# Optimization experiments

Measured on AMD Instinct MI355X. Metric: run time of the kernel, lower is better.

The kernel has to match this reference:

```python
import jax, jax.numpy as jnp
import numpy as np

H = 16       # num attention heads
HKV = 4      # num key/value heads
HD = 128     # head dim
EPS = 1e-6
ROPE_BASE = 10000.0


def _rms_norm(x, w):
    # per-head RMSNorm over last dim (head_dim), computed in fp32
    xf = x.astype(jnp.float32)
    var = jnp.mean(xf * xf, axis=-1, keepdims=True)
    return (w * (xf * jax.lax.rsqrt(var + EPS))).astype(x.dtype)


def _rotate_half(x):
    x1, x2 = jnp.split(x, 2, axis=-1)
    return jnp.concatenate((-x2, x1), axis=-1)


def _rope_cos_sin(position_ids, dtype):
    inv_freq = 1.0 / (ROPE_BASE ** (jnp.arange(0, HD, 2, dtype=jnp.float32) / HD))
    freqs = position_ids.astype(jnp.float32)[..., None] * inv_freq  # [B,S,HD/2]
    emb = jnp.concatenate((freqs, freqs), axis=-1)                  # [B,S,HD]
    return jnp.cos(emb).astype(dtype), jnp.sin(emb).astype(dtype)


def setup_inputs() -> dict:
    key = jax.random.key(0)
    ks = jax.random.split(key, 6)
    B, S, D = 2, 2048, 2048
    return {
        "hidden_states": jax.random.normal(ks[0], (B, S, D), jnp.float32),
        "wq": jax.random.normal(ks[1], (D, H * HD), jnp.float32) * 0.02,
        "wk": jax.random.normal(ks[2], (D, HKV * HD), jnp.float32) * 0.02,
        "wv": jax.random.normal(ks[3], (D, HKV * HD), jnp.float32) * 0.02,
        "wo": jax.random.normal(ks[4], (H * HD, D), jnp.float32) * 0.02,
        "q_norm_w": jnp.ones((HD,), jnp.float32),
        "k_norm_w": jnp.ones((HD,), jnp.float32),
        "position_ids": jnp.tile(jnp.arange(S, dtype=jnp.int32)[None, :], (B, 1)),
    }


def reference(hidden_states, wq, wk, wv, wo, q_norm_w, k_norm_w, position_ids):
    B, S, D = hidden_states.shape
    # projections + per-head q/k RMSNorm (Qwen3)
    q = _rms_norm(jnp.einsum("bsd,de->bse", hidden_states, wq).reshape(B, S, H, HD), q_norm_w)
    k = _rms_norm(jnp.einsum("bsd,de->bse", hidden_states, wk).reshape(B, S, HKV, HD), k_norm_w)
    v = jnp.einsum("bsd,de->bse", hidden_states, wv).reshape(B, S, HKV, HD)
    # [B, H, S, HD]
    q = q.transpose(0, 2, 1, 3)
    k = k.transpose(0, 2, 1, 3)
    v = v.transpose(0, 2, 1, 3)
    # RoPE (cos/sin broadcast over head dim, unsqueeze_dim=1)
    cos, sin = _rope_cos_sin(position_ids, q.dtype)
    cos, sin = cos[:, None], sin[:, None]
    q = q * cos + _rotate_half(q) * sin
    k = k * cos + _rotate_half(k) * sin
    # GQA repeat_kv: [B,HKV,S,HD] -> [B,H,S,HD]
    n_rep = H // HKV
    k = jnp.repeat(k, n_rep, axis=1)
    v = jnp.repeat(v, n_rep, axis=1)
    # SDPA, causal
    scale = 1.0 / jnp.sqrt(jnp.asarray(HD, q.dtype))
    scores = jnp.einsum("bhqd,bhkd->bhqk", q, k) * scale
    causal = jnp.tril(jnp.ones((S, S), bool))
    scores = jnp.where(causal, scores, jnp.asarray(-1e9, scores.dtype))
    attn = jax.nn.softmax(scores, axis=-1)
    out = jnp.einsum("bhqk,bhkd->bhqd", attn, v)         # [B,H,S,HD]
    out = out.transpose(0, 2, 1, 3).reshape(B, S, H * HD)
    return jnp.einsum("bse,ed->bsd", out, wo)
```

## Files before the change

kernel.cpp:

```cpp
#include <hip/hip_runtime.h>
#include <hip/hip_bf16.h>
#include <cstddef>

constexpr int B_   = 2;
constexpr int S_   = 2048;
constexpr int D_   = 2048;
constexpr int H_   = 16;
constexpr int HKV_ = 4;
constexpr int HD_  = 128;
constexpr int M_   = B_ * S_;
constexpr int NQKV_ = H_ * HD_ + 2 * HKV_ * HD_;
constexpr float QSCALE = 0.08838834764831845f;

typedef __attribute__((ext_vector_type(8))) short bs8;
typedef __attribute__((ext_vector_type(4))) float fx4;

__device__ __forceinline__ void split2(float x, short& hi, short& lo) {
  __hip_bfloat16 h = __float2bfloat16(x);
  float hf = __bfloat162float(h);
  __hip_bfloat16 l = __float2bfloat16(x - hf);
  hi = *(short*)&h;
  lo = *(short*)&l;
}

__device__ __forceinline__ void gload16(const short* g, short* l) {
  __builtin_amdgcn_global_load_lds(
      (const __attribute__((address_space(1))) void*)g,
      (__attribute__((address_space(3))) void*)l, 16, 0, 0);
}

__global__ __launch_bounds__(256) void split_hidden(
    const float4* __restrict__ X, short* __restrict__ out)
{
  const long i4  = (long)blockIdx.x * 256 + threadIdx.x;
  const long row = i4 >> 9;
  const long c   = (i4 & 511) * 4;
  const float4 v = X[i4];
  short h[4], l[4];
  split2(v.x, h[0], l[0]); split2(v.y, h[1], l[1]);
  split2(v.z, h[2], l[2]); split2(v.w, h[3], l[3]);
  *(short4*)&out[row * 4096 + c]        = make_short4(h[0], h[1], h[2], h[3]);
  *(short4*)&out[row * 4096 + 2048 + c] = make_short4(l[0], l[1], l[2], l[3]);
}

__global__ __launch_bounds__(256) void tsplit(
    const float* __restrict__ W, int N, short* __restrict__ out, int row0)
{
  __shared__ float tile[32][33];
  const int k0 = blockIdx.y * 32;
  const int n0 = blockIdx.x * 32;
  const int x = threadIdx.x, y = threadIdx.y;
  #pragma unroll
  for (int i = 0; i < 4; ++i)
    tile[y + 8 * i][x] = W[(size_t)(k0 + y + 8 * i) * N + n0 + x];
  __syncthreads();
  #pragma unroll
  for (int i = 0; i < 4; ++i) {
    const int n = n0 + y + 8 * i;
    const float v = tile[x][y + 8 * i];
    short hi, lo;
    split2(v, hi, lo);
    out[(size_t)(row0 + n) * 4096 + k0 + x]        = hi;
    out[(size_t)(row0 + n) * 4096 + 2048 + k0 + x] = lo;
  }
}

__global__ __launch_bounds__(256, 2) void gemm_split_bf16(
    const short* __restrict__ Asp, const short* __restrict__ Bsp,
    float* __restrict__ C, int M, int N, int K)
{
  __shared__ short As[128 * 32];
  __shared__ short Bs[128 * 32];

  const int t    = threadIdx.x;
  const int lane = t & 63, wid = t >> 6;
  const int wr   = wid >> 1, wc = wid & 1;
  const int bm   = blockIdx.y * 128, bn = blockIdx.x * 128;
  const int ld   = 2 * K;

  fx4 acc[4][4] = {};

  const int sr = t >> 2;
  const int sk = (t & 3) * 8;
  short* lA  = As + t * 8;
  short* lA2 = As + (t + 256) * 8;
  short* lB  = Bs + t * 8;
  short* lB2 = Bs + (t + 256) * 8;
  const short* gA = Asp + (size_t)(bm + sr) * ld + sk;
  const short* gB = Bsp + (size_t)(bn + sr) * ld + sk;
  const size_t rstep = (size_t)64 * ld;

  const int lr = lane & 15, lk = (lane >> 4) * 8;

  for (int kp = 0; kp < 3 * K; kp += 32) {
    const int ca = (kp < 2 * K) ? kp : kp - 2 * K;
    const int cb = (kp < K) ? kp : kp - K;
    gload16(gA + ca, lA);
    gload16(gA + ca + rstep, lA2);
    gload16(gB + cb, lB);
    gload16(gB + cb + rstep, lB2);
    __syncthreads();

    bs8 af[4], bf[4];
    #pragma unroll
    for (int m = 0; m < 4; ++m)
      af[m] = *(const bs8*)&As[(wr * 64 + m * 16 + lr) * 32 + lk];
    #pragma unroll
    for (int n = 0; n < 4; ++n)
      bf[n] = *(const bs8*)&Bs[(wc * 64 + n * 16 + lr) * 32 + lk];
    #pragma unroll
    for (int m = 0; m < 4; ++m)
      #pragma unroll
      for (int n = 0; n < 4; ++n)
        acc[m][n] = __builtin_amdgcn_mfma_f32_16x16x32_bf16(af[m], bf[n], acc[m][n], 0, 0, 0);
    __syncthreads();
  }

  const int lg = lane >> 4;
  #pragma unroll
  for (int m = 0; m < 4; ++m)
    #pragma unroll
    for (int n = 0; n < 4; ++n) {
      const int col = bn + wc * 64 + n * 16 + lr;
      #pragma unroll
      for (int r = 0; r < 4; ++r) {
        const int row = bm + wr * 64 + m * 16 + lg * 4 + r;
        C[(size_t)row * N + col] = acc[m][n][r];
      }
    }
}

__global__ __launch_bounds__(64) void rmsrope(
    float* __restrict__ qkv, const float* __restrict__ qw,
    const float* __restrict__ kw, const int* __restrict__ pos_ids)
{
  const int row  = blockIdx.x;
  const int lane = threadIdx.x;
  constexpr int NQROWS = M_ * H_;
  const bool isq = row < NQROWS;

  int token; float* ptr; const float* w;
  if (isq) {
    token = row / H_;
    ptr = qkv + (size_t)token * NQKV_ + (row % H_) * HD_;
    w = qw;
  } else {
    const int rk = row - NQROWS;
    token = rk / HKV_;
    ptr = qkv + (size_t)token * NQKV_ + 2048 + (rk % HKV_) * HD_;
    w = kw;
  }

  const float x1 = ptr[lane];
  const float x2 = ptr[lane + 64];
  float ss = x1 * x1 + x2 * x2;
  #pragma unroll
  for (int m = 1; m < 64; m <<= 1) ss += __shfl_xor(ss, m, 64);
  const float rinv = rsqrtf(ss * (1.0f / 128.0f) + 1e-6f);
  const float y1 = x1 * rinv * w[lane];
  const float y2 = x2 * rinv * w[lane + 64];

  const int pos = pos_ids[token];
  const float f = (float)pos * powf(10000.0f, -(float)lane * (1.0f / 64.0f));
  float sn, c;
  sincosf(f, &sn, &c);
  const float o1 = y1 * c - y2 * sn;
  const float o2 = y2 * c + y1 * sn;

  if (isq) {
    ptr[lane]      = o1;
    ptr[lane + 64] = o2;
  } else {
    short* srow = (short*)ptr;
    short h1, l1, h2, l2;
    split2(o1, h1, l1);
    split2(o2, h2, l2);
    srow[lane]       = h1;  srow[lane + 64]  = h2;
    srow[128 + lane] = l1;  srow[192 + lane] = l2;
  }
}

__global__ __launch_bounds__(256) void vtrans(
    const float* __restrict__ qkv, short* __restrict__ vsp)
{
  __shared__ float tile[32][33];
  const int by = blockIdx.y;
  const int b = by >> 4, kvh = (by >> 2) & 3, d0 = (by & 3) * 32;
  const int s0 = blockIdx.x * 32;
  const int tx = threadIdx.x, ty = threadIdx.y;
  #pragma unroll
  for (int i = 0; i < 4; ++i)
    tile[ty + 8 * i][tx] =
        qkv[(size_t)(b * S_ + s0 + ty + 8 * i) * NQKV_ + 2560 + kvh * 128 + d0 + tx];
  __syncthreads();
  #pragma unroll
  for (int i = 0; i < 4; ++i) {
    const int d = d0 + ty + 8 * i;
    __hip_bfloat16 v = __float2bfloat16(tile[tx][ty + 8 * i]);
    vsp[((size_t)(b * HKV_ + kvh) * 128 + d) * (size_t)S_ + s0 + tx] = *(short*)&v;
  }
}

__global__ __launch_bounds__(256, 2) void attn_mfma(
    const float* __restrict__ qkv, const short* __restrict__ vsp,
    short* __restrict__ osp)
{
  __shared__ __align__(16) short Kh[64 * 128];
  __shared__ __align__(16) short Kl[64 * 128];
  __shared__ __align__(16) short Vt[128 * 64];
  __shared__ __align__(16) short sP[64 * 64];

  const int t    = threadIdx.x;
  const int lane = t & 63;
  const int w    = t >> 6;
  const int lr   = lane & 15;
  const int g    = lane >> 4;
  const int qt = blockIdx.x, bh = blockIdx.y;
  const int b = bh >> 4, h = bh & 15;
  const int kvh = h >> 2;
  const int q0  = qt * 64;
  const int bhk = b * HKV_ + kvh;
  const short* kb = (const short*)qkv;

  bs8 qh[4], ql[4];
  {
    const float* qrow = qkv + (size_t)(b * S_ + q0 + 16 * w + lr) * NQKV_ + h * HD_ + g * 8;
    #pragma unroll
    for (int dc = 0; dc < 4; ++dc) {
      float x[8];
      *(float4*)&x[0] = *(const float4*)(qrow + 32 * dc);
      *(float4*)&x[4] = *(const float4*)(qrow + 32 * dc + 4);
      #pragma unroll
      for (int i = 0; i < 8; ++i) {
        short hi, lo;
        split2(x[i] * QSCALE, hi, lo);
        qh[dc][i] = hi; ql[dc][i] = lo;
      }
    }
  }

  fx4 o[8] = {};
  float m_i[4] = {-1e30f, -1e30f, -1e30f, -1e30f};
  float l_i[4] = {0.f, 0.f, 0.f, 0.f};

  const int sj = t >> 2, sq = t & 3;
  const int vd = t >> 1, vjh = t & 1;

  for (int kt = 0; kt <= qt; ++kt) {
    const int k0 = kt * 64;
    __syncthreads();

    {
      const short* krow = kb + (size_t)(b * S_ + k0 + sj) * 6144 + 4096 + kvh * 256 + 32 * sq;
      const short* vrow = vsp + ((size_t)bhk * 128 + vd) * (size_t)S_ + k0 + 32 * vjh;
      #pragma unroll
      for (int ci = 0; ci < 4; ++ci) {
        const int kblk = (((4 * sq + ci) ^ (sj & 15)) << 3);
        *(bs8*)&Kh[sj * 128 + kblk] = *(const bs8*)(krow + 8 * ci);
        *(bs8*)&Kl[sj * 128 + kblk] = *(const bs8*)(krow + 128 + 8 * ci);
        *(bs8*)&Vt[vd * 64 + ((((4 * vjh + ci) ^ (vd & 7))) << 3)] = *(const bs8*)(vrow + 8 * ci);
      }
    }
    __syncthreads();

    fx4 s[4] = {};
    #pragma unroll
    for (int dc = 0; dc < 4; ++dc) {
      #pragma unroll
      for (int n = 0; n < 4; ++n) {
        const int ko = (16 * n + lr) * 128 + (((dc * 4 + g) ^ lr) << 3);
        const bs8 fh = *(const bs8*)&Kh[ko];
        const bs8 fl = *(const bs8*)&Kl[ko];
        s[n] = __builtin_amdgcn_mfma_f32_16x16x32_bf16(qh[dc], fh, s[n], 0, 0, 0);
        s[n] = __builtin_amdgcn_mfma_f32_16x16x32_bf16(ql[dc], fh, s[n], 0, 0, 0);
        s[n] = __builtin_amdgcn_mfma_f32_16x16x32_bf16(qh[dc], fl, s[n], 0, 0, 0);
      }
    }

    if (kt == qt) {
      #pragma unroll
      for (int n = 0; n < 4; ++n)
        #pragma unroll
        for (int r = 0; r < 4; ++r)
          if (16 * n + lr > 16 * w + 4 * g + r) s[n][r] = -1e30f;
    }

    #pragma unroll
    for (int r = 0; r < 4; ++r) {
      float rm = fmaxf(fmaxf(s[0][r], s[1][r]), fmaxf(s[2][r], s[3][r]));
      rm = fmaxf(rm, __shfl_xor(rm, 1, 64));
      rm = fmaxf(rm, __shfl_xor(rm, 2, 64));
      rm = fmaxf(rm, __shfl_xor(rm, 4, 64));
      rm = fmaxf(rm, __shfl_xor(rm, 8, 64));
      const float mn    = fmaxf(m_i[r], rm);
      const float alpha = __expf(m_i[r] - mn);
      float ps = 0.f;
      #pragma unroll
      for (int n = 0; n < 4; ++n) {
        const float p = __expf(s[n][r] - mn);
        s[n][r] = p;
        ps += p;
      }
      ps += __shfl_xor(ps, 1, 64);
      ps += __shfl_xor(ps, 2, 64);
      ps += __shfl_xor(ps, 4, 64);
      ps += __shfl_xor(ps, 8, 64);
      l_i[r] = l_i[r] * alpha + ps;
      m_i[r] = mn;
      #pragma unroll
      for (int df = 0; df < 8; ++df) o[df][r] *= alpha;

      const int rr = 16 * w + 4 * g + r;
      #pragma unroll
      for (int n = 0; n < 4; ++n) {
        __hip_bfloat16 pb = __float2bfloat16(s[n][r]);
        sP[rr * 64 + ((((2 * n + (lr >> 3)) ^ (rr & 7))) << 3) + (lr & 7)] = *(short*)&pb;
      }
    }

    const int pro = (16 * w + lr) * 64;
    const bs8 pa0 = *(const bs8*)&sP[pro + (((g)     ^ (lr & 7)) << 3)];
    const bs8 pa1 = *(const bs8*)&sP[pro + (((g + 4) ^ (lr & 7)) << 3)];
    #pragma unroll
    for (int df = 0; df < 8; ++df) {
      const int vo = (16 * df + lr) * 64;
      const bs8 v0 = *(const bs8*)&Vt[vo + (((g)     ^ (lr & 7)) << 3)];
      const bs8 v1 = *(const bs8*)&Vt[vo + (((g + 4) ^ (lr & 7)) << 3)];
      o[df] = __builtin_amdgcn_mfma_f32_16x16x32_bf16(pa0, v0, o[df], 0, 0, 0);
      o[df] = __builtin_amdgcn_mfma_f32_16x16x32_bf16(pa1, v1, o[df], 0, 0, 0);
    }
  }

  #pragma unroll
  for (int r = 0; r < 4; ++r) {
    const float inv = 1.0f / l_i[r];
    const size_t ro = (size_t)(b * S_ + q0 + 16 * w + 4 * g + r) * 4096 + h * HD_;
    #pragma unroll
    for (int df = 0; df < 8; ++df) {
      short hi, lo;
      split2(o[df][r] * inv, hi, lo);
      osp[ro + 16 * df + lr]        = hi;
      osp[ro + 2048 + 16 * df + lr] = lo;
    }
  }
}

extern "C" void kernel_launch(void* const* d_in, const int* in_sizes, int n_in,
                              void* d_out, int out_size, void* d_ws, size_t ws_size,
                              hipStream_t stream) {
  const float* hidden = (const float*)d_in[0];
  const float* wq     = (const float*)d_in[1];
  const float* wk     = (const float*)d_in[2];
  const float* wv     = (const float*)d_in[3];
  const float* wo     = (const float*)d_in[4];
  const float* qw     = (const float*)d_in[5];
  const float* kw     = (const float*)d_in[6];
  const int*   pos    = (const int*)d_in[7];
  float*       out    = (float*)d_out;

  const size_t aspB = (size_t)M_ * 4096 * 2;
  const size_t bspB = (size_t)NQKV_ * 4096 * 2;
  const size_t qkvB = (size_t)M_ * NQKV_ * 4;
  if (ws_size < aspB + bspB + qkvB) return;

  short* Asp = (short*)d_ws;
  short* Bsp = (short*)((char*)d_ws + aspB);
  float* qkv = (float*)((char*)d_ws + aspB + bspB);
  short* Osp = Asp;
  short* Vsp = Bsp + (size_t)2048 * 4096;

  split_hidden<<<(M_ * D_ / 4) / 256, 256, 0, stream>>>((const float4*)hidden, Asp);
  tsplit<<<dim3(2048 / 32, 64), dim3(32, 8), 0, stream>>>(wq, 2048, Bsp, 0);
  tsplit<<<dim3(512 / 32, 64),  dim3(32, 8), 0, stream>>>(wk, 512,  Bsp, 2048);
  tsplit<<<dim3(512 / 32, 64),  dim3(32, 8), 0, stream>>>(wv, 512,  Bsp, 2560);

  gemm_split_bf16<<<dim3(NQKV_ / 128, M_ / 128), 256, 0, stream>>>(
      Asp, Bsp, qkv, M_, NQKV_, 2048);

  rmsrope<<<M_ * (H_ + HKV_), 64, 0, stream>>>(qkv, qw, kw, pos);

  vtrans<<<dim3(S_ / 32, 32), dim3(32, 8), 0, stream>>>(qkv, Vsp);

  attn_mfma<<<dim3(S_ / 64, B_ * H_), 256, 0, stream>>>(qkv, Vsp, Osp);

  tsplit<<<dim3(2048 / 32, 64), dim3(32, 8), 0, stream>>>(wo, 2048, Bsp, 0);
  gemm_split_bf16<<<dim3(D_ / 128, M_ / 128), 256, 0, stream>>>(
      Osp, Bsp, out, M_, D_, 2048);
}
```

Measured before the change: 674.2 us.

## Restructure attention with 128-row tiles, double-buffered async K/V loads, causal pairing

The attention kernel now processes 128 query rows per block, two 16-row sub-tiles per wave, which reuses each K/V fragment read from LDS across more MFMAs. K/V tiles are double-buffered and fetched straight into LDS with global_load_lds under manual vmcnt waits and raw barriers, so the next tile's load overlaps the current tile's compute. Each block handles a light and a heavy causal query tile (p and 15-p) to even out work, and the grid becomes 8x32 blocks. The GEMM also remaps block ids in a strided pattern to improve L2 locality. In exchange, LDS use and register pressure go up and occupancy drops to one block per SM, and the grid has only 256 blocks.

```diff
diff --git a/kernel.cpp b/kernel.cpp
--- a/kernel.cpp
+++ b/kernel.cpp
@@ -29,6 +29,16 @@
       (__attribute__((address_space(3))) void*)l, 16, 0, 0);
 }
 
+__device__ __forceinline__ void bar_raw() {
+  asm volatile("s_barrier" ::: "memory");
+}
+__device__ __forceinline__ void vmwait12() {
+  asm volatile("s_waitcnt vmcnt(12)" ::: "memory");
+}
+__device__ __forceinline__ void vmwait0() {
+  asm volatile("s_waitcnt vmcnt(0)" ::: "memory");
+}
+
 __global__ __launch_bounds__(256) void split_hidden(
     const float4* __restrict__ X, short* __restrict__ out)
 {
@@ -75,8 +85,13 @@
   const int t    = threadIdx.x;
   const int lane = t & 63, wid = t >> 6;
   const int wr   = wid >> 1, wc = wid & 1;
-  const int bm   = blockIdx.y * 128, bn = blockIdx.x * 128;
-  const int ld   = 2 * K;
+
+  const int nbx = gridDim.x;
+  const int nwg = nbx * gridDim.y;
+  int bid = blockIdx.y * nbx + blockIdx.x;
+  bid = (bid & 7) * (nwg >> 3) + (bid >> 3);
+  const int bm = (bid / nbx) * 128, bn = (bid % nbx) * 128;
+  const int ld = 2 * K;
 
   fx4 acc[4][4] = {};
 
@@ -201,147 +216,212 @@
   }
 }
 
-__global__ __launch_bounds__(256, 2) void attn_mfma(
+__global__ __launch_bounds__(256, 1) void attn_mfma2(
     const float* __restrict__ qkv, const short* __restrict__ vsp,
     short* __restrict__ osp)
 {
-  __shared__ __align__(16) short Kh[64 * 128];
-  __shared__ __align__(16) short Kl[64 * 128];
-  __shared__ __align__(16) short Vt[128 * 64];
-  __shared__ __align__(16) short sP[64 * 64];
+  __shared__ __align__(16) short KhB[2][64 * 128];
+  __shared__ __align__(16) short KlB[2][64 * 128];
+  __shared__ __align__(16) short VtB[2][128 * 64];
+  __shared__ __align__(16) short sP[128 * 64];
 
   const int t    = threadIdx.x;
   const int lane = t & 63;
   const int w    = t >> 6;
   const int lr   = lane & 15;
   const int g    = lane >> 4;
-  const int qt = blockIdx.x, bh = blockIdx.y;
+  const int p  = blockIdx.x;
+  const int bh = blockIdx.y;
   const int b = bh >> 4, h = bh & 15;
   const int kvh = h >> 2;
-  const int q0  = qt * 64;
   const int bhk = b * HKV_ + kvh;
   const short* kb = (const short*)qkv;
 
-  bs8 qh[4], ql[4];
-  {
-    const float* qrow = qkv + (size_t)(b * S_ + q0 + 16 * w + lr) * NQKV_ + h * HD_ + g * 8;
-    #pragma unroll
-    for (int dc = 0; dc < 4; ++dc) {
-      float x[8];
-      *(float4*)&x[0] = *(const float4*)(qrow + 32 * dc);
-      *(float4*)&x[4] = *(const float4*)(qrow + 32 * dc + 4);
-      #pragma unroll
-      for (int i = 0; i < 8; ++i) {
-        short hi, lo;
-        split2(x[i] * QSCALE, hi, lo);
-        qh[dc][i] = hi; ql[dc][i] = lo;
+  const int kidx[4] = {w * 256 + 0 * 64 + lane, w * 256 + 1 * 64 + lane,
+                       w * 256 + 2 * 64 + lane, w * 256 + 3 * 64 + lane};
+
+  const int qts[2] = {p, 15 - p};
+
+  #pragma unroll 1
+  for (int sg = 0; sg < 2; ++sg) {
+    const int qt  = qts[sg];
+    const int q0  = 128 * qt;
+    const int ntk = 2 * qt + 2;
+
+    bs8 qh[2][4], ql[2][4];
+    #pragma unroll
+    for (int m = 0; m < 2; ++m) {
+      const float* qrow =
+          qkv + (size_t)(b * S_ + q0 + 32 * w + 16 * m + lr) * NQKV_ + h * HD_ + g * 8;
+      #pragma unroll
+      for (int dc = 0; dc < 4; ++dc) {
+        float x[8];
+        *(float4*)&x[0] = *(const float4*)(qrow + 32 * dc);
+        *(float4*)&x[4] = *(const float4*)(qrow + 32 * dc + 4);
+        #pragma unroll
+        for (int e = 0; e < 8; ++e) {
+          short hi, lo;
+          split2(x[e] * QSCALE, hi, lo);
+          qh[m][dc][e] = hi; ql[m][dc][e] = lo;
+        }
       }
     }
-  }
-
-  fx4 o[8] = {};
-  float m_i[4] = {-1e30f, -1e30f, -1e30f, -1e30f};
-  float l_i[4] = {0.f, 0.f, 0.f, 0.f};
-
-  const int sj = t >> 2, sq = t & 3;
-  const int vd = t >> 1, vjh = t & 1;
-
-  for (int kt = 0; kt <= qt; ++kt) {
-    const int k0 = kt * 64;
-    __syncthreads();
+
+    fx4 o[2][8] = {};
+    float m_i[2][4], l_i[2][4];
+    #pragma unroll
+    for (int m = 0; m < 2; ++m)
+      #pragma unroll
+      for (int r = 0; r < 4; ++r) { m_i[m][r] = -1e30f; l_i[m][r] = 0.f; }
 
     {
-      const short* krow = kb + (size_t)(b * S_ + k0 + sj) * 6144 + 4096 + kvh * 256 + 32 * sq;
-      const short* vrow = vsp + ((size_t)bhk * 128 + vd) * (size_t)S_ + k0 + 32 * vjh;
-      #pragma unroll
-      for (int ci = 0; ci < 4; ++ci) {
-        const int kblk = (((4 * sq + ci) ^ (sj & 15)) << 3);
-        *(bs8*)&Kh[sj * 128 + kblk] = *(const bs8*)(krow + 8 * ci);
-        *(bs8*)&Kl[sj * 128 + kblk] = *(const bs8*)(krow + 128 + 8 * ci);
-        *(bs8*)&Vt[vd * 64 + ((((4 * vjh + ci) ^ (vd & 7))) << 3)] = *(const bs8*)(vrow + 8 * ci);
+      const int k0 = 0;
+      #pragma unroll
+      for (int i = 0; i < 4; ++i) {
+        const int idx = kidx[i];
+        const int sj = idx >> 4, cc = idx & 15;
+        const short* kr = kb + (size_t)(b * S_ + k0 + sj) * 6144 + 4096 + kvh * 256;
+        gload16(kr + 8 * (cc ^ (sj & 15)), &KhB[0][(w * 4 + i) * 512]);
+        gload16(kr + 128 + 8 * (cc ^ (sj & 15)), &KlB[0][(w * 4 + i) * 512]);
+        const int d = idx >> 3, c2 = idx & 7;
+        const short* vr = vsp + ((size_t)bhk * 128 + d) * (size_t)S_ + k0;
+        gload16(vr + 8 * (c2 ^ (d & 7)), &VtB[0][(w * 4 + i) * 512]);
       }
     }
-    __syncthreads();
-
-    fx4 s[4] = {};
-    #pragma unroll
-    for (int dc = 0; dc < 4; ++dc) {
-      #pragma unroll
-      for (int n = 0; n < 4; ++n) {
-        const int ko = (16 * n + lr) * 128 + (((dc * 4 + g) ^ lr) << 3);
-        const bs8 fh = *(const bs8*)&Kh[ko];
-        const bs8 fl = *(const bs8*)&Kl[ko];
-        s[n] = __builtin_amdgcn_mfma_f32_16x16x32_bf16(qh[dc], fh, s[n], 0, 0, 0);
-        s[n] = __builtin_amdgcn_mfma_f32_16x16x32_bf16(ql[dc], fh, s[n], 0, 0, 0);
-        s[n] = __builtin_amdgcn_mfma_f32_16x16x32_bf16(qh[dc], fl, s[n], 0, 0, 0);
-      }
+    vmwait0();
+    bar_raw();
+
+    int buf = 0;
+    #pragma unroll 1
+    for (int kt = 0; kt < ntk; ++kt) {
+      const int k0 = 64 * kt;
+
+      if (kt + 1 < ntk) {
+        const int kn = 64 * (kt + 1);
+        #pragma unroll
+        for (int i = 0; i < 4; ++i) {
+          const int idx = kidx[i];
+          const int sj = idx >> 4, cc = idx & 15;
+          const short* kr = kb + (size_t)(b * S_ + kn + sj) * 6144 + 4096 + kvh * 256;
+          gload16(kr + 8 * (cc ^ (sj & 15)), &KhB[buf ^ 1][(w * 4 + i) * 512]);
+          gload16(kr + 128 + 8 * (cc ^ (sj & 15)), &KlB[buf ^ 1][(w * 4 + i) * 512]);
+          const int d = idx >> 3, c2 = idx & 7;
+          const short* vr = vsp + ((size_t)bhk * 128 + d) * (size_t)S_ + kn;
+          gload16(vr + 8 * (c2 ^ (d & 7)), &VtB[buf ^ 1][(w * 4 + i) * 512]);
+        }
+        vmwait12();
+      } else {
+        vmwait0();
+      }
+      bar_raw();
+
+      const short* Kh = KhB[buf];
+      const short* Kl = KlB[buf];
+      const short* Vt = VtB[buf];
+
+      fx4 s[2][4] = {};
+      #pragma unroll
+      for (int dc = 0; dc < 4; ++dc) {
+        #pragma unroll
+        for (int n = 0; n < 4; ++n) {
+          const int ko = (16 * n + lr) * 128 + (((dc * 4 + g) ^ lr) << 3);
+          const bs8 fh = *(const bs8*)&Kh[ko];
+          const bs8 fl = *(const bs8*)&Kl[ko];
+          #pragma unroll
+          for (int m = 0; m < 2; ++m) {
+            s[m][n] = __builtin_amdgcn_mfma_f32_16x16x32_bf16(qh[m][dc], fh, s[m][n], 0, 0, 0);
+            s[m][n] = __builtin_amdgcn_mfma_f32_16x16x32_bf16(ql[m][dc], fh, s[m][n], 0, 0, 0);
+            s[m][n] = __builtin_amdgcn_mfma_f32_16x16x32_bf16(qh[m][dc], fl, s[m][n], 0, 0, 0);
+          }
+        }
+      }
+
+      if (k0 + 64 > q0) {
+        #pragma unroll
+        for (int m = 0; m < 2; ++m)
+          #pragma unroll
+          for (int n = 0; n < 4; ++n)
+            #pragma unroll
+            for (int r = 0; r < 4; ++r)
+              if (k0 + 16 * n + lr > q0 + 32 * w + 16 * m + 4 * g + r)
+                s[m][n][r] = -1e30f;
+      }
+
+      #pragma unroll
+      for (int m = 0; m < 2; ++m) {
+        #pragma unroll
+        for (int r = 0; r < 4; ++r) {
+          float rm = fmaxf(fmaxf(s[m][0][r], s[m][1][r]),
+                           fmaxf(s[m][2][r], s[m][3][r]));
+          rm = fmaxf(rm, __shfl_xor(rm, 1, 64));
+          rm = fmaxf(rm, __shfl_xor(rm, 2, 64));
+          rm = fmaxf(rm, __shfl_xor(rm, 4, 64));
+          rm = fmaxf(rm, __shfl_xor(rm, 8, 64));
+          const float mn    = fmaxf(m_i[m][r], rm);
+          const float alpha = __expf(m_i[m][r] - mn);
+          float ps = 0.f;
+          #pragma unroll
+          for (int n = 0; n < 4; ++n) {
+            const float pv = __expf(s[m][n][r] - mn);
+            s[m][n][r] = pv;
+            ps += pv;
+          }
+          ps += __shfl_xor(ps, 1, 64);
+          ps += __shfl_xor(ps, 2, 64);
+          ps += __shfl_xor(ps, 4, 64);
+          ps += __shfl_xor(ps, 8, 64);
+          l_i[m][r] = l_i[m][r] * alpha + ps;
+          m_i[m][r] = mn;
+          #pragma unroll
+          for (int df = 0; df < 8; ++df) o[m][df][r] *= alpha;
+
+          const int rr = 32 * w + 16 * m + 4 * g + r;
+          #pragma unroll
+          for (int n = 0; n < 4; ++n) {
+            __hip_bfloat16 pb = __float2bfloat16(s[m][n][r]);
+            sP[rr * 64 + ((((2 * n + (lr >> 3)) ^ (rr & 7))) << 3) + (lr & 7)] = *(short*)&pb;
+          }
+        }
+      }
+
+      bs8 pa[2][2];
+      #pragma unroll
+      for (int m = 0; m < 2; ++m) {
+        const int pro = (32 * w + 16 * m + lr) * 64;
+        pa[m][0] = *(const bs8*)&sP[pro + (((g)     ^ (lr & 7)) << 3)];
+        pa[m][1] = *(const bs8*)&sP[pro + (((g + 4) ^ (lr & 7)) << 3)];
+      }
+      #pragma unroll
+      for (int df = 0; df < 8; ++df) {
+        const int vo = (16 * df + lr) * 64;
+        const bs8 v0 = *(const bs8*)&Vt[vo + (((g)     ^ (lr & 7)) << 3)];
+        const bs8 v1 = *(const bs8*)&Vt[vo + (((g + 4) ^ (lr & 7)) << 3)];
+        #pragma unroll
+        for (int m = 0; m < 2; ++m) {
+          o[m][df] = __builtin_amdgcn_mfma_f32_16x16x32_bf16(pa[m][0], v0, o[m][df], 0, 0, 0);
+          o[m][df] = __builtin_amdgcn_mfma_f32_16x16x32_bf16(pa[m][1], v1, o[m][df], 0, 0, 0);
+        }
+      }
+
+      bar_raw();
+      buf ^= 1;
     }
 
-    if (kt == qt) {
-      #pragma unroll
-      for (int n = 0; n < 4; ++n)
-        #pragma unroll
-        for (int r = 0; r < 4; ++r)
-          if (16 * n + lr > 16 * w + 4 * g + r) s[n][r] = -1e30f;
-    }
-
-    #pragma unroll
-    for (int r = 0; r < 4; ++r) {
-      float rm = fmaxf(fmaxf(s[0][r], s[1][r]), fmaxf(s[2][r], s[3][r]));
-      rm = fmaxf(rm, __shfl_xor(rm, 1, 64));
-      rm = fmaxf(rm, __shfl_xor(rm, 2, 64));
-      rm = fmaxf(rm, __shfl_xor(rm, 4, 64));
-      rm = fmaxf(rm, __shfl_xor(rm, 8, 64));
-      const float mn    = fmaxf(m_i[r], rm);
-      const float alpha = __expf(m_i[r] - mn);
-      float ps = 0.f;
-      #pragma unroll
-      for (int n = 0; n < 4; ++n) {
-        const float p = __expf(s[n][r] - mn);
-        s[n][r] = p;
-        ps += p;
-      }
-      ps += __shfl_xor(ps, 1, 64);
-      ps += __shfl_xor(ps, 2, 64);
-      ps += __shfl_xor(ps, 4, 64);
-      ps += __shfl_xor(ps, 8, 64);
-      l_i[r] = l_i[r] * alpha + ps;
-      m_i[r] = mn;
-      #pragma unroll
-      for (int df = 0; df < 8; ++df) o[df][r] *= alpha;
-
-      const int rr = 16 * w + 4 * g + r;
-      #pragma unroll
-      for (int n = 0; n < 4; ++n) {
-        __hip_bfloat16 pb = __float2bfloat16(s[n][r]);
-        sP[rr * 64 + ((((2 * n + (lr >> 3)) ^ (rr & 7))) << 3) + (lr & 7)] = *(short*)&pb;
-      }
-    }
-
-    const int pro = (16 * w + lr) * 64;
-    const bs8 pa0 = *(const bs8*)&sP[pro + (((g)     ^ (lr & 7)) << 3)];
-    const bs8 pa1 = *(const bs8*)&sP[pro + (((g + 4) ^ (lr & 7)) << 3)];
-    #pragma unroll
-    for (int df = 0; df < 8; ++df) {
-      const int vo = (16 * df + lr) * 64;
-      const bs8 v0 = *(const bs8*)&Vt[vo + (((g)     ^ (lr & 7)) << 3)];
-      const bs8 v1 = *(const bs8*)&Vt[vo + (((g + 4) ^ (lr & 7)) << 3)];
-      o[df] = __builtin_amdgcn_mfma_f32_16x16x32_bf16(pa0, v0, o[df], 0, 0, 0);
-      o[df] = __builtin_amdgcn_mfma_f32_16x16x32_bf16(pa1, v1, o[df], 0, 0, 0);
-    }
-  }
-
-  #pragma unroll
-  for (int r = 0; r < 4; ++r) {
-    const float inv = 1.0f / l_i[r];
-    const size_t ro = (size_t)(b * S_ + q0 + 16 * w + 4 * g + r) * 4096 + h * HD_;
-    #pragma unroll
-    for (int df = 0; df < 8; ++df) {
-      short hi, lo;
-      split2(o[df][r] * inv, hi, lo);
-      osp[ro + 16 * df + lr]        = hi;
-      osp[ro + 2048 + 16 * df + lr] = lo;
-    }
+    #pragma unroll
+    for (int m = 0; m < 2; ++m)
+      #pragma unroll
+      for (int r = 0; r < 4; ++r) {
+        const float inv = 1.0f / l_i[m][r];
+        const size_t ro =
+            (size_t)(b * S_ + q0 + 32 * w + 16 * m + 4 * g + r) * 4096 + h * HD_;
+        #pragma unroll
+        for (int df = 0; df < 8; ++df) {
+          short hi, lo;
+          split2(o[m][df][r] * inv, hi, lo);
+          osp[ro + 16 * df + lr]        = hi;
+          osp[ro + 2048 + 16 * df + lr] = lo;
+        }
+      }
   }
 }
 
@@ -381,7 +461,7 @@
 
   vtrans<<<dim3(S_ / 32, 32), dim3(32, 8), 0, stream>>>(qkv, Vsp);
 
-  attn_mfma<<<dim3(S_ / 64, B_ * H_), 256, 0, stream>>>(qkv, Vsp, Osp);
+  attn_mfma2<<<dim3(8, B_ * H_), 256, 0, stream>>>(qkv, Vsp, Osp);
 
   tsplit<<<dim3(2048 / 32, 64), dim3(32, 8), 0, stream>>>(wo, 2048, Bsp, 0);
   gemm_split_bf16<<<dim3(D_ / 128, M_ / 128), 256, 0, stream>>>(
```

Result: faster. 633.1 us (-6.1%).

## Pair causal q-tiles per block, register-prefetch K/V, swizzle GEMM block order

Applied to the files above, without the earlier changes.

The attention kernel now gives each block two query tiles (p and 31-p) so every block gets the same causal work. It also prefetches the next K/V tile into registers while the current tile is being computed, so global loads overlap the MFMA work. MFMA sections are wrapped in s_setprio to raise wave priority. The GEMM remaps block IDs with an XCD-style interleave (bid&7) to improve L2 locality across dies. The costs are extra register pressure from the prefetch buffers and half as many attention blocks in the grid.

```diff
diff --git a/kernel.cpp b/kernel.cpp
--- a/kernel.cpp
+++ b/kernel.cpp
@@ -75,8 +75,13 @@
   const int t    = threadIdx.x;
   const int lane = t & 63, wid = t >> 6;
   const int wr   = wid >> 1, wc = wid & 1;
-  const int bm   = blockIdx.y * 128, bn = blockIdx.x * 128;
-  const int ld   = 2 * K;
+
+  const int nbx = gridDim.x;
+  const int nwg = nbx * gridDim.y;
+  int bid = blockIdx.y * nbx + blockIdx.x;
+  bid = (bid & 7) * (nwg >> 3) + (bid >> 3);
+  const int bm = (bid / nbx) * 128, bn = (bid % nbx) * 128;
+  const int ld = 2 * K;
 
   fx4 acc[4][4] = {};
 
@@ -201,7 +206,7 @@
   }
 }
 
-__global__ __launch_bounds__(256, 2) void attn_mfma(
+__global__ __launch_bounds__(256, 2) void attn_mfma3(
     const float* __restrict__ qkv, const short* __restrict__ vsp,
     short* __restrict__ osp)
 {
@@ -215,132 +220,172 @@
   const int w    = t >> 6;
   const int lr   = lane & 15;
   const int g    = lane >> 4;
-  const int qt = blockIdx.x, bh = blockIdx.y;
+  const int p  = blockIdx.x;
+  const int bh = blockIdx.y;
   const int b = bh >> 4, h = bh & 15;
   const int kvh = h >> 2;
-  const int q0  = qt * 64;
   const int bhk = b * HKV_ + kvh;
   const short* kb = (const short*)qkv;
 
-  bs8 qh[4], ql[4];
-  {
-    const float* qrow = qkv + (size_t)(b * S_ + q0 + 16 * w + lr) * NQKV_ + h * HD_ + g * 8;
-    #pragma unroll
-    for (int dc = 0; dc < 4; ++dc) {
-      float x[8];
-      *(float4*)&x[0] = *(const float4*)(qrow + 32 * dc);
-      *(float4*)&x[4] = *(const float4*)(qrow + 32 * dc + 4);
-      #pragma unroll
-      for (int i = 0; i < 8; ++i) {
+  bs8 rKh[4], rKl[4], rV[4];
+
+  const short* kbase = kb + (size_t)b * S_ * 6144 + 4096 + kvh * 256;
+  const short* vbase = vsp + (size_t)bhk * 128 * (size_t)S_;
+
+  auto stage_load = [&](int k0) {
+    #pragma unroll
+    for (int i = 0; i < 4; ++i) {
+      const int idx = t + 256 * i;
+      const int sj = idx >> 4, c = idx & 15;
+      rKh[i] = *(const bs8*)(kbase + (size_t)(k0 + sj) * 6144 + 8 * c);
+      rKl[i] = *(const bs8*)(kbase + (size_t)(k0 + sj) * 6144 + 128 + 8 * c);
+      const int d = idx >> 3, c2 = idx & 7;
+      rV[i] = *(const bs8*)(vbase + (size_t)d * S_ + k0 + 8 * c2);
+    }
+  };
+  auto stage_write = [&]() {
+    #pragma unroll
+    for (int i = 0; i < 4; ++i) {
+      const int idx = t + 256 * i;
+      const int sj = idx >> 4, c = idx & 15;
+      *(bs8*)&Kh[sj * 128 + ((c ^ (sj & 15)) << 3)] = rKh[i];
+      *(bs8*)&Kl[sj * 128 + ((c ^ (sj & 15)) << 3)] = rKl[i];
+      const int d = idx >> 3, c2 = idx & 7;
+      *(bs8*)&Vt[d * 64 + ((c2 ^ (d & 7)) << 3)] = rV[i];
+    }
+  };
+
+  const int qts[2] = {p, 31 - p};
+
+  #pragma unroll 1
+  for (int sg = 0; sg < 2; ++sg) {
+    const int qt  = qts[sg];
+    const int q0  = 64 * qt;
+    const int ntk = qt + 1;
+
+    stage_load(0);
+
+    bs8 qh[4], ql[4];
+    {
+      const float* qrow =
+          qkv + (size_t)(b * S_ + q0 + 16 * w + lr) * NQKV_ + h * HD_ + g * 8;
+      #pragma unroll
+      for (int dc = 0; dc < 4; ++dc) {
+        float x[8];
+        *(float4*)&x[0] = *(const float4*)(qrow + 32 * dc);
+        *(float4*)&x[4] = *(const float4*)(qrow + 32 * dc + 4);
+        #pragma unroll
+        for (int e = 0; e < 8; ++e) {
+          short hi, lo;
+          split2(x[e] * QSCALE, hi, lo);
+          qh[dc][e] = hi; ql[dc][e] = lo;
+        }
+      }
+    }
+
+    fx4 o[8] = {};
+    float m_i[4] = {-1e30f, -1e30f, -1e30f, -1e30f};
+    float l_i[4] = {0.f, 0.f, 0.f, 0.f};
+
+    stage_write();
+    __syncthreads();
+    if (ntk > 1) stage_load(64);
+
+    #pragma unroll 1
+    for (int kt = 0; kt < ntk; ++kt) {
+      const int k0 = 64 * kt;
+
+      fx4 s[4] = {};
+      __builtin_amdgcn_s_setprio(1);
+      #pragma unroll
+      for (int dc = 0; dc < 4; ++dc) {
+        #pragma unroll
+        for (int n = 0; n < 4; ++n) {
+          const int ko = (16 * n + lr) * 128 + (((dc * 4 + g) ^ lr) << 3);
+          const bs8 fh = *(const bs8*)&Kh[ko];
+          const bs8 fl = *(const bs8*)&Kl[ko];
+          s[n] = __builtin_amdgcn_mfma_f32_16x16x32_bf16(qh[dc], fh, s[n], 0, 0, 0);
+          s[n] = __builtin_amdgcn_mfma_f32_16x16x32_bf16(ql[dc], fh, s[n], 0, 0, 0);
+          s[n] = __builtin_amdgcn_mfma_f32_16x16x32_bf16(qh[dc], fl, s[n], 0, 0, 0);
+        }
+      }
+      __builtin_amdgcn_s_setprio(0);
+
+      if (kt == qt) {
+        #pragma unroll
+        for (int n = 0; n < 4; ++n)
+          #pragma unroll
+          for (int r = 0; r < 4; ++r)
+            if (16 * n + lr > 16 * w + 4 * g + r) s[n][r] = -1e30f;
+      }
+
+      #pragma unroll
+      for (int r = 0; r < 4; ++r) {
+        float rm = fmaxf(fmaxf(s[0][r], s[1][r]), fmaxf(s[2][r], s[3][r]));
+        rm = fmaxf(rm, __shfl_xor(rm, 1, 64));
+        rm = fmaxf(rm, __shfl_xor(rm, 2, 64));
+        rm = fmaxf(rm, __shfl_xor(rm, 4, 64));
+        rm = fmaxf(rm, __shfl_xor(rm, 8, 64));
+        const float mn    = fmaxf(m_i[r], rm);
+        const float alpha = __expf(m_i[r] - mn);
+        float ps = 0.f;
+        #pragma unroll
+        for (int n = 0; n < 4; ++n) {
+          const float pv = __expf(s[n][r] - mn);
+          s[n][r] = pv;
+          ps += pv;
+        }
+        ps += __shfl_xor(ps, 1, 64);
+        ps += __shfl_xor(ps, 2, 64);
+        ps += __shfl_xor(ps, 4, 64);
+        ps += __shfl_xor(ps, 8, 64);
+        l_i[r] = l_i[r] * alpha + ps;
+        m_i[r] = mn;
+        #pragma unroll
+        for (int df = 0; df < 8; ++df) o[df][r] *= alpha;
+
+        const int rr = 16 * w + 4 * g + r;
+        #pragma unroll
+        for (int n = 0; n < 4; ++n) {
+          __hip_bfloat16 pb = __float2bfloat16(s[n][r]);
+          sP[rr * 64 + ((((2 * n + (lr >> 3)) ^ (rr & 7))) << 3) + (lr & 7)] = *(short*)&pb;
+        }
+      }
+
+      const int pro = (16 * w + lr) * 64;
+      const bs8 pa0 = *(const bs8*)&sP[pro + (((g)     ^ (lr & 7)) << 3)];
+      const bs8 pa1 = *(const bs8*)&sP[pro + (((g + 4) ^ (lr & 7)) << 3)];
+      __builtin_amdgcn_s_setprio(1);
+      #pragma unroll
+      for (int df = 0; df < 8; ++df) {
+        const int vo = (16 * df + lr) * 64;
+        const bs8 v0 = *(const bs8*)&Vt[vo + (((g)     ^ (lr & 7)) << 3)];
+        const bs8 v1 = *(const bs8*)&Vt[vo + (((g + 4) ^ (lr & 7)) << 3)];
+        o[df] = __builtin_amdgcn_mfma_f32_16x16x32_bf16(pa0, v0, o[df], 0, 0, 0);
+        o[df] = __builtin_amdgcn_mfma_f32_16x16x32_bf16(pa1, v1, o[df], 0, 0, 0);
+      }
+      __builtin_amdgcn_s_setprio(0);
+
+      __syncthreads();
+      if (kt + 1 < ntk) {
+        stage_write();
+        __syncthreads();
+        if (kt + 2 < ntk) stage_load(64 * (kt + 2));
+      }
+    }
+
+    #pragma unroll
+    for (int r = 0; r < 4; ++r) {
+      const float inv = 1.0f / l_i[r];
+      const size_t ro =
+          (size_t)(b * S_ + q0 + 16 * w + 4 * g + r) * 4096 + h * HD_;
+      #pragma unroll
+      for (int df = 0; df < 8; ++df) {
         short hi, lo;
-        split2(x[i] * QSCALE, hi, lo);
-        qh[dc][i] = hi; ql[dc][i] = lo;
-      }
-    }
-  }
-
-  fx4 o[8] = {};
-  float m_i[4] = {-1e30f, -1e30f, -1e30f, -1e30f};
-  float l_i[4] = {0.f, 0.f, 0.f, 0.f};
-
-  const int sj = t >> 2, sq = t & 3;
-  const int vd = t >> 1, vjh = t & 1;
-
-  for (int kt = 0; kt <= qt; ++kt) {
-    const int k0 = kt * 64;
-    __syncthreads();
-
-    {
-      const short* krow = kb + (size_t)(b * S_ + k0 + sj) * 6144 + 4096 + kvh * 256 + 32 * sq;
-      const short* vrow = vsp + ((size_t)bhk * 128 + vd) * (size_t)S_ + k0 + 32 * vjh;
-      #pragma unroll
-      for (int ci = 0; ci < 4; ++ci) {
-        const int kblk = (((4 * sq + ci) ^ (sj & 15)) << 3);
-        *(bs8*)&Kh[sj * 128 + kblk] = *(const bs8*)(krow + 8 * ci);
-        *(bs8*)&Kl[sj * 128 + kblk] = *(const bs8*)(krow + 128 + 8 * ci);
-        *(bs8*)&Vt[vd * 64 + ((((4 * vjh + ci) ^ (vd & 7))) << 3)] = *(const bs8*)(vrow + 8 * ci);
-      }
-    }
-    __syncthreads();
-
-    fx4 s[4] = {};
-    #pragma unroll
-    for (int dc = 0; dc < 4; ++dc) {
-      #pragma unroll
-      for (int n = 0; n < 4; ++n) {
-        const int ko = (16 * n + lr) * 128 + (((dc * 4 + g) ^ lr) << 3);
-        const bs8 fh = *(const bs8*)&Kh[ko];
-        const bs8 fl = *(const bs8*)&Kl[ko];
-        s[n] = __builtin_amdgcn_mfma_f32_16x16x32_bf16(qh[dc], fh, s[n], 0, 0, 0);
-        s[n] = __builtin_amdgcn_mfma_f32_16x16x32_bf16(ql[dc], fh, s[n], 0, 0, 0);
-        s[n] = __builtin_amdgcn_mfma_f32_16x16x32_bf16(qh[dc], fl, s[n], 0, 0, 0);
-      }
-    }
-
-    if (kt == qt) {
-      #pragma unroll
-      for (int n = 0; n < 4; ++n)
-        #pragma unroll
-        for (int r = 0; r < 4; ++r)
-          if (16 * n + lr > 16 * w + 4 * g + r) s[n][r] = -1e30f;
-    }
-
-    #pragma unroll
-    for (int r = 0; r < 4; ++r) {
-      float rm = fmaxf(fmaxf(s[0][r], s[1][r]), fmaxf(s[2][r], s[3][r]));
-      rm = fmaxf(rm, __shfl_xor(rm, 1, 64));
-      rm = fmaxf(rm, __shfl_xor(rm, 2, 64));
-      rm = fmaxf(rm, __shfl_xor(rm, 4, 64));
-      rm = fmaxf(rm, __shfl_xor(rm, 8, 64));
-      const float mn    = fmaxf(m_i[r], rm);
-      const float alpha = __expf(m_i[r] - mn);
-      float ps = 0.f;
-      #pragma unroll
-      for (int n = 0; n < 4; ++n) {
-        const float p = __expf(s[n][r] - mn);
-        s[n][r] = p;
-        ps += p;
-      }
-      ps += __shfl_xor(ps, 1, 64);
-      ps += __shfl_xor(ps, 2, 64);
-      ps += __shfl_xor(ps, 4, 64);
-      ps += __shfl_xor(ps, 8, 64);
-      l_i[r] = l_i[r] * alpha + ps;
-      m_i[r] = mn;
-      #pragma unroll
-      for (int df = 0; df < 8; ++df) o[df][r] *= alpha;
-
-      const int rr = 16 * w + 4 * g + r;
-      #pragma unroll
-      for (int n = 0; n < 4; ++n) {
-        __hip_bfloat16 pb = __float2bfloat16(s[n][r]);
-        sP[rr * 64 + ((((2 * n + (lr >> 3)) ^ (rr & 7))) << 3) + (lr & 7)] = *(short*)&pb;
-      }
-    }
-
-    const int pro = (16 * w + lr) * 64;
-    const bs8 pa0 = *(const bs8*)&sP[pro + (((g)     ^ (lr & 7)) << 3)];
-    const bs8 pa1 = *(const bs8*)&sP[pro + (((g + 4) ^ (lr & 7)) << 3)];
-    #pragma unroll
-    for (int df = 0; df < 8; ++df) {
-      const int vo = (16 * df + lr) * 64;
-      const bs8 v0 = *(const bs8*)&Vt[vo + (((g)     ^ (lr & 7)) << 3)];
-      const bs8 v1 = *(const bs8*)&Vt[vo + (((g + 4) ^ (lr & 7)) << 3)];
-      o[df] = __builtin_amdgcn_mfma_f32_16x16x32_bf16(pa0, v0, o[df], 0, 0, 0);
-      o[df] = __builtin_amdgcn_mfma_f32_16x16x32_bf16(pa1, v1, o[df], 0, 0, 0);
-    }
-  }
-
-  #pragma unroll
-  for (int r = 0; r < 4; ++r) {
-    const float inv = 1.0f / l_i[r];
-    const size_t ro = (size_t)(b * S_ + q0 + 16 * w + 4 * g + r) * 4096 + h * HD_;
-    #pragma unroll
-    for (int df = 0; df < 8; ++df) {
-      short hi, lo;
-      split2(o[df][r] * inv, hi, lo);
-      osp[ro + 16 * df + lr]        = hi;
-      osp[ro + 2048 + 16 * df + lr] = lo;
+        split2(o[df][r] * inv, hi, lo);
+        osp[ro + 16 * df + lr]        = hi;
+        osp[ro + 2048 + 16 * df + lr] = lo;
+      }
     }
   }
 }
@@ -381,7 +426,7 @@
 
   vtrans<<<dim3(S_ / 32, 32), dim3(32, 8), 0, stream>>>(qkv, Vsp);
 
-  attn_mfma<<<dim3(S_ / 64, B_ * H_), 256, 0, stream>>>(qkv, Vsp, Osp);
+  attn_mfma3<<<dim3(16, B_ * H_), 256, 0, stream>>>(qkv, Vsp, Osp);
 
   tsplit<<<dim3(2048 / 32, 64), dim3(32, 8), 0, stream>>>(wo, 2048, Bsp, 0);
   gemm_split_bf16<<<dim3(D_ / 128, M_ / 128), 256, 0, stream>>>(
```

New measurement: 594.5 us. 1.13x faster.
